# Kernel tuning notes

Measured on AMD Instinct MI355X. Metric: run time of the kernel, lower is better.

## Reference

```python
import jax, jax.numpy as jnp
import numpy as np

NEG_SLOPE = 0.2  # PyG GATv2Conv default negative_slope


def setup_inputs() -> dict:
    key = jax.random.key(0)
    ks = jax.random.split(key, 8)
    B, N, C, H, F, E = 16, 5000, 128, 2, 64, 1_280_000
    T = B * N
    s = 0.05
    x = jax.random.normal(ks[0], (B, N, C), jnp.float32)
    edge_index = jax.random.randint(ks[1], (2, E), 0, T, jnp.int32)
    Wl = jax.random.normal(ks[2], (C, H * F), jnp.float32) * s
    bl = jnp.zeros((H * F,), jnp.float32)
    Wr = jax.random.normal(ks[3], (C, H * F), jnp.float32) * s
    br = jnp.zeros((H * F,), jnp.float32)
    att = jax.random.normal(ks[4], (H, F), jnp.float32) * s
    bias = jnp.zeros((H * F,), jnp.float32)
    return {"x": x, "edge_index": edge_index, "Wl": Wl, "bl": bl,
            "Wr": Wr, "br": br, "att": att, "bias": bias}


def reference(x, edge_index, Wl, bl, Wr, br, att, bias):
    # x: (B, N, C) -> flatten to (T, C), T = B*N total nodes
    B, N, C = x.shape
    T = B * N
    H, F = att.shape
    xf = x.reshape(T, C)
    x_l = (xf @ Wl + bl).reshape(T, H, F)  # source transform (lin_l)
    x_r = (xf @ Wr + br).reshape(T, H, F)  # target transform (lin_r)
    # add self loops (add_self_loops=True)
    loops = jnp.arange(T, dtype=edge_index.dtype)
    src = jnp.concatenate([edge_index[0], loops])
    dst = jnp.concatenate([edge_index[1], loops])
    # GATv2 score: att . LeakyReLU(x_j + x_i)
    e = jax.nn.leaky_relu(x_l[src] + x_r[dst], NEG_SLOPE)  # (Et, H, F)
    logits = jnp.einsum('ehf,hf->eh', e, att)              # (Et, H)
    # edge softmax over incoming edges of each dst node
    m = jax.lax.stop_gradient(jax.ops.segment_max(logits, dst, num_segments=T))
    p = jnp.exp(logits - m[dst])
    denom = jax.ops.segment_sum(p, dst, num_segments=T)
    alpha = p / denom[dst]                                  # (Et, H)
    # aggregate: out_i = sum_j alpha_ij * x_l[j]
    out = jax.ops.segment_sum(x_l[src] * alpha[:, :, None], dst, num_segments=T)
    out = out.reshape(T, H * F) + bias  # concat=True -> (T, H*F)
    return out.reshape(B, N, H * F)
```

## Files before the change

kernel.cpp:

```cpp
#include <hip/hip_runtime.h>
#include <hip/hip_bf16.h>

typedef __hip_bfloat16 bf16;
typedef short s16x8 __attribute__((ext_vector_type(8)));
typedef float f32x4 __attribute__((ext_vector_type(4)));
typedef float f32x2 __attribute__((ext_vector_type(2)));

#define NEG_SLOPE 0.2f
#define MAXB 160
#define EPB  4096
#define CAP  12288

__device__ __forceinline__ unsigned int f32_to_bf16_bits(float f) {
    unsigned int u = __float_as_uint(f);
    return (u + 0x7FFFu + ((u >> 16) & 1u)) >> 16;
}
__device__ __forceinline__ float bf16lo_to_f32(unsigned int u) {
    return __uint_as_float(u << 16);
}
__device__ __forceinline__ float bf16hi_to_f32(unsigned int u) {
    return __uint_as_float(u & 0xFFFF0000u);
}
__device__ __forceinline__ float loadf_rt(const void* p, size_t i, int isb) {
    return isb ? __bfloat162float(((const bf16*)p)[i]) : ((const float*)p)[i];
}

#define ROR_ADD(v, n)                                                          \
    v += __int_as_float(__builtin_amdgcn_update_dpp(                           \
        0, __float_as_int(v), 0x120 + (n), 0xF, 0xF, true))

__global__ void prep_w(const unsigned short* __restrict__ xh,
                       const void* __restrict__ Wl, const void* __restrict__ Wr,
                       unsigned short* __restrict__ bpack,
                       int* __restrict__ flag, int* __restrict__ gtot)
{
    if (blockIdx.x == 16) {
        int tid = threadIdx.x;
        for (int j = tid; j < MAXB; j += 256) gtot[j] = 0;
        unsigned short h = xh[tid & 255];
        int e = (h >> 7) & 0xFF;
        int c = ((h & 0x7FFF) == 0 || (e >= 117 && e <= 131)) ? 1 : 0;
        __shared__ int sc[4];
        int lane = tid & 63, wid = tid >> 6;
        #pragma unroll
        for (int off = 32; off; off >>= 1) c += __shfl_xor(c, off, 64);
        if (lane == 0) sc[wid] = c;
        __syncthreads();
        if (tid == 0) *flag = ((sc[0] + sc[1] + sc[2] + sc[3]) >= 4 * 192) ? 1 : 0;
        return;
    }

    __shared__ int s_isb;
    {
        int tl = threadIdx.x;
        if (tl < 64) {
            int cnt = 0;
            for (int j = tl; j < 256; j += 64) {
                unsigned short h = xh[j];
                int e = (h >> 7) & 0xFF;
                if ((h & 0x7FFF) == 0 || (e >= 117 && e <= 131)) cnt++;
            }
            #pragma unroll
            for (int off = 32; off; off >>= 1) cnt += __shfl_xor(cnt, off, 64);
            if (tl == 0) s_isb = (cnt >= 192) ? 1 : 0;
        }
        __syncthreads();
    }
    int isb = s_isb;

    int tid = blockIdx.x * 256 + threadIdx.x;
    int lane = tid & 63;
    int kc   = (tid >> 6) & 3;
    int nt   = (tid >> 8) & 7;
    int mat  = tid >> 11;
    const void* W = mat ? Wr : Wl;
    int n  = nt * 16 + (lane & 15);
    int k0 = kc * 32 + (lane >> 4) * 8;
    unsigned short* o = bpack + (size_t)tid * 8;
    #pragma unroll
    for (int j = 0; j < 8; ++j)
        o[j] = (unsigned short)f32_to_bf16_bits(loadf_rt(W, (size_t)(k0 + j) * 128 + n, isb));
}

__global__ void gemm_or_hist(const void* __restrict__ x,
                             const unsigned short* __restrict__ bpack,
                             const void* __restrict__ bl, const void* __restrict__ br,
                             unsigned int* __restrict__ xlp, unsigned int* __restrict__ xrp,
                             int T, const int* __restrict__ flag,
                             const int* __restrict__ ei, int E, int Et,
                             int nbuck, int Gg, int* __restrict__ gtot)
{
    __shared__ int h[4][MAXB];

    if ((int)blockIdx.x >= Gg) {
        int hb  = blockIdx.x - Gg;
        int tid = threadIdx.x, wid = tid >> 6;
        for (int j = tid; j < 4 * MAXB; j += 256) h[j / MAXB][j % MAXB] = 0;
        __syncthreads();
        int start = hb * EPB;
        int end   = min(start + EPB, Et);
        for (int i = start + tid; i < end; i += 256) {
            int dst = (i < E) ? ei[E + i] : (i - E);
            atomicAdd(&h[wid][dst >> 9], 1);
        }
        __syncthreads();
        for (int b = tid; b < nbuck; b += 256) {
            int v = h[0][b] + h[1][b] + h[2][b] + h[3][b];
            if (v) atomicAdd(&gtot[b], v);
        }
        return;
    }

    int isb  = *flag;
    int lane = threadIdx.x & 63;
    int w    = blockIdx.x * 4 + (threadIdx.x >> 6);
    int row0 = w * 16;
    if (row0 >= T) return;
    int m = lane & 15, quad = lane >> 4;
    int arow = min(row0 + m, T - 1);

    f32x4 acc[16];
    #pragma unroll
    for (int nt = 0; nt < 16; ++nt) acc[nt] = (f32x4){0.f, 0.f, 0.f, 0.f};

    const s16x8* bp = (const s16x8*)bpack;
    for (int kc = 0; kc < 4; ++kc) {
        s16x8 a;
        if (isb) {
            const unsigned short* xb = (const unsigned short*)x
                                     + (size_t)arow * 128 + kc * 32 + quad * 8;
            a = *(const s16x8*)xb;
        } else {
            const float* xp = (const float*)x + (size_t)arow * 128 + kc * 32 + quad * 8;
            float4 xa = ((const float4*)xp)[0];
            float4 xc = ((const float4*)xp)[1];
            a[0] = (short)f32_to_bf16_bits(xa.x); a[1] = (short)f32_to_bf16_bits(xa.y);
            a[2] = (short)f32_to_bf16_bits(xa.z); a[3] = (short)f32_to_bf16_bits(xa.w);
            a[4] = (short)f32_to_bf16_bits(xc.x); a[5] = (short)f32_to_bf16_bits(xc.y);
            a[6] = (short)f32_to_bf16_bits(xc.z); a[7] = (short)f32_to_bf16_bits(xc.w);
        }
        #pragma unroll
        for (int nt = 0; nt < 16; ++nt) {
            s16x8 b = bp[(size_t)(((nt >> 3) * 32) + (nt & 7) * 4 + kc) * 64 + lane];
            acc[nt] = __builtin_amdgcn_mfma_f32_16x16x32_bf16(a, b, acc[nt], 0, 0, 0);
        }
    }
    #pragma unroll
    for (int nt = 0; nt < 4; ++nt) {
        int fl = nt * 16 + m;
        float bl0 = loadf_rt(bl, fl, isb), bl1 = loadf_rt(bl, 64 + fl, isb);
        float br0 = loadf_rt(br, fl, isb), br1 = loadf_rt(br, 64 + fl, isb);
        #pragma unroll
        for (int r = 0; r < 4; ++r) {
            int t = row0 + quad * 4 + r;
            if (t < T) {
                unsigned int pl = f32_to_bf16_bits(acc[nt][r] + bl0)
                                | (f32_to_bf16_bits(acc[nt + 4][r] + bl1) << 16);
                unsigned int pr = f32_to_bf16_bits(acc[nt + 8][r] + br0)
                                | (f32_to_bf16_bits(acc[nt + 12][r] + br1) << 16);
                xlp[(size_t)t * 64 + fl] = pl;
                xrp[(size_t)t * 64 + fl] = pr;
            }
        }
    }
}

__global__ void scan_buckets(int* __restrict__ gtot, int nbuck, int Et,
                             int* __restrict__ bases, int* __restrict__ rowptr_T)
{
    __shared__ int sd[256];
    int tid = threadIdx.x;
    int v = (tid < nbuck) ? gtot[tid] : 0;
    sd[tid] = v;
    __syncthreads();
    for (int off = 1; off < 256; off <<= 1) {
        int u = (tid >= off) ? sd[tid - off] : 0;
        __syncthreads();
        sd[tid] += u;
        __syncthreads();
    }
    int excl = sd[tid] - v;
    if (tid < nbuck) { bases[tid] = excl; gtot[tid] = excl; }
    if (tid == 0) { bases[nbuck] = Et; *rowptr_T = Et; }
}

__global__ void bucket_scatter2(const int* __restrict__ ei, int E, int Et,
                                int nbuck, int* __restrict__ gcur,
                                unsigned int* __restrict__ packed)
{
    __shared__ int h[4][MAXB];
    __shared__ int cur[MAXB];
    int tid = threadIdx.x, wid = tid >> 6;
    for (int j = tid; j < 4 * MAXB; j += 256) h[j / MAXB][j % MAXB] = 0;
    __syncthreads();
    int start = blockIdx.x * EPB;
    int end   = min(start + EPB, Et);
    for (int i = start + tid; i < end; i += 256) {
        int dst = (i < E) ? ei[E + i] : (i - E);
        atomicAdd(&h[wid][dst >> 9], 1);
    }
    __syncthreads();
    for (int b = tid; b < nbuck; b += 256) {
        int v = h[0][b] + h[1][b] + h[2][b] + h[3][b];
        cur[b] = v ? atomicAdd(&gcur[b], v) : 0;
    }
    __syncthreads();
    for (int i = start + tid; i < end; i += 256) {
        int src, dst;
        if (i < E) { src = ei[i]; dst = ei[E + i]; }
        else       { src = i - E; dst = i - E; }
        int pos = atomicAdd(&cur[dst >> 9], 1);
        packed[pos] = ((unsigned int)src << 9) | (unsigned int)(dst & 511);
    }
}

__global__ void build_csr(unsigned int* __restrict__ colpacked,
                          const int* __restrict__ bases, int nbuck,
                          int Et, int T, int* __restrict__ row_ptr)
{
    __shared__ unsigned int st[CAP];
    __shared__ int h[512];
    __shared__ int off[512];
    __shared__ int ws[4];
    int b    = blockIdx.x;
    int tid  = threadIdx.x, lane = tid & 63, wid = tid >> 6;
    int base = bases[b];
    int endb = bases[b + 1];
    int m    = min(endb - base, CAP);

    for (int i = tid; i < m; i += 256) st[i] = colpacked[base + i];
    for (int j = tid; j < 512; j += 256) h[j] = 0;
    __syncthreads();
    for (int i = tid; i < m; i += 256) atomicAdd(&h[st[i] & 511], 1);
    __syncthreads();

    int h0 = h[2 * tid], h1 = h[2 * tid + 1];
    int s  = h0 + h1;
    int xx = s;
    #pragma unroll
    for (int o = 1; o < 64; o <<= 1) {
        int u = __shfl_up(xx, o, 64);
        if (lane >= o) xx += u;
    }
    if (lane == 63) ws[wid] = xx;
    __syncthreads();
    int wo = 0;
    for (int wv = 0; wv < 4; ++wv) if (wv < wid) wo += ws[wv];
    int e0 = wo + xx - s;
    int e1 = e0 + h0;
    off[2 * tid]     = e0;
    off[2 * tid + 1] = e1;
    int node0 = b * 512 + 2 * tid;
    if (node0 < T)     row_ptr[node0]     = base + e0;
    if (node0 + 1 < T) row_ptr[node0 + 1] = base + e1;
    __syncthreads();

    for (int i = tid; i < m; i += 256) {
        unsigned int p = st[i];
        int pos = atomicAdd(&off[p & 511], 1);
        colpacked[base + pos] = p >> 9;
    }
}

__global__ void aggregate(const unsigned int* __restrict__ xlp,
                          const unsigned int* __restrict__ xrp,
                          const int* __restrict__ row_ptr, const int* __restrict__ col,
                          const void* __restrict__ att, const void* __restrict__ bias,
                          float* __restrict__ out, int T,
                          const int* __restrict__ flag)
{
    int lane = threadIdx.x & 63;
    int node = blockIdx.x * 8 + (threadIdx.x >> 5);
    if (node >= T) return;
    int isb = *flag;
    int g = (lane >> 4) & 1;
    int q = lane & 15;

    uint4 xr4 = ((const uint4*)(xrp + (size_t)node * 64))[q];
    f32x2 xr2[4], at2[4];
    {
        unsigned int xrw[4] = {xr4.x, xr4.y, xr4.z, xr4.w};
        const float LOG2E = 1.44269504f;
        #pragma unroll
        for (int k = 0; k < 4; ++k) {
            xr2[k] = (f32x2){bf16lo_to_f32(xrw[k]), bf16hi_to_f32(xrw[k])};
            at2[k] = (f32x2){loadf_rt(att, q * 4 + k, isb) * LOG2E,
                             loadf_rt(att, 64 + q * 4 + k, isb) * LOG2E};
        }
    }

    f32x2 s2 = {0.f, 0.f};
    f32x2 a2[4] = {{0.f, 0.f}, {0.f, 0.f}, {0.f, 0.f}, {0.f, 0.f}};

    int beg = row_ptr[node], end = row_ptr[node + 1];

    bool v0 = (beg + g) < end;      int sA = v0 ? col[beg + g]     : node;
    bool v1 = (beg + 2 + g) < end;  int sB = v1 ? col[beg + 2 + g] : node;
    bool v2 = (beg + 4 + g) < end;  int sC = v2 ? col[beg + 4 + g] : node;
    uint4 cx = ((const uint4*)(xlp + (size_t)sA * 64))[q];
    uint4 nx = ((const uint4*)(xlp + (size_t)sB * 64))[q];

    for (int i = beg; i < end; i += 2) {
        bool v3 = (i + 6 + g) < end;
        int  sD = v3 ? col[i + 6 + g] : node;
        uint4 px = ((const uint4*)(xlp + (size_t)sC * 64))[q];

        unsigned int xlw[4] = {cx.x, cx.y, cx.z, cx.w};
        f32x2 xl2[4];
        f32x2 t2 = {0.f, 0.f};
        #pragma unroll
        for (int k = 0; k < 4; ++k) {
            xl2[k] = (f32x2){bf16lo_to_f32(xlw[k]), bf16hi_to_f32(xlw[k])};
            f32x2 e  = xl2[k] + xr2[k];
            f32x2 lr = __builtin_elementwise_max(e, e * NEG_SLOPE);
            t2 = __builtin_elementwise_fma(lr, at2[k], t2);
        }
        float t0 = t2.x, t1 = t2.y;
        ROR_ADD(t0, 8); ROR_ADD(t1, 8);
        ROR_ADD(t0, 4); ROR_ADD(t1, 4);
        ROR_ADD(t0, 2); ROR_ADD(t1, 2);
        ROR_ADD(t0, 1); ROR_ADD(t1, 1);
        t0 = fminf(t0, 43.3f);
        t1 = fminf(t1, 43.3f);
        f32x2 p2;
        p2.x = v0 ? exp2f(t0) : 0.f;
        p2.y = v0 ? exp2f(t1) : 0.f;
        s2 += p2;
        #pragma unroll
        for (int k = 0; k < 4; ++k)
            a2[k] = __builtin_elementwise_fma(p2, xl2[k], a2[k]);

        cx = nx; nx = px;
        v0 = v1; v1 = v2; v2 = v3; sC = sD;
    }

    s2.x += __shfl_xor(s2.x, 16, 64);
    s2.y += __shfl_xor(s2.y, 16, 64);
    #pragma unroll
    for (int k = 0; k < 4; ++k) {
        a2[k].x += __shfl_xor(a2[k].x, 16, 64);
        a2[k].y += __shfl_xor(a2[k].y, 16, 64);
    }

    float inv0 = (s2.x > 0.f) ? 1.f / s2.x : 0.f;
    float inv1 = (s2.y > 0.f) ? 1.f / s2.y : 0.f;
    if (g == 0) {
        float4 o;
        o.x = fmaf(a2[0].x, inv0, loadf_rt(bias, q * 4 + 0, isb));
        o.y = fmaf(a2[1].x, inv0, loadf_rt(bias, q * 4 + 1, isb));
        o.z = fmaf(a2[2].x, inv0, loadf_rt(bias, q * 4 + 2, isb));
        o.w = fmaf(a2[3].x, inv0, loadf_rt(bias, q * 4 + 3, isb));
        ((float4*)(out + (size_t)node * 128))[q] = o;
    } else {
        float4 o;
        o.x = fmaf(a2[0].y, inv1, loadf_rt(bias, 64 + q * 4 + 0, isb));
        o.y = fmaf(a2[1].y, inv1, loadf_rt(bias, 64 + q * 4 + 1, isb));
        o.z = fmaf(a2[2].y, inv1, loadf_rt(bias, 64 + q * 4 + 2, isb));
        o.w = fmaf(a2[3].y, inv1, loadf_rt(bias, 64 + q * 4 + 3, isb));
        ((float4*)(out + (size_t)node * 128))[16 + q] = o;
    }
}

extern "C" void kernel_launch(void* const* d_in, const int* in_sizes, int n_in,
                              void* d_out, int out_size, void* d_ws, size_t ws_size,
                              hipStream_t stream)
{
    const void* x    = d_in[0];
    const int*  ei   = (const int*)d_in[1];
    const void* Wl   = d_in[2];
    const void* bl   = d_in[3];
    const void* Wr   = d_in[4];
    const void* br   = d_in[5];
    const void* att  = d_in[6];
    const void* bias = d_in[7];
    float* out = (float*)d_out;

    int T     = in_sizes[0] / 128;
    int E     = in_sizes[1] / 2;
    int Et    = E + T;
    int nbuck = (T + 511) >> 9;
    int nb    = (Et + EPB - 1) / EPB;
    int Gg    = (T + 63) / 64;

    char* w = (char*)d_ws;
    unsigned int* xlp = (unsigned int*)w;  w += (size_t)T * 64 * 4;
    unsigned int* xrp = (unsigned int*)w;  w += (size_t)T * 64 * 4;
    int* rowptr = (int*)w;  w += (size_t)(T + 1) * 4;
    unsigned int* col = (unsigned int*)w;  w += (size_t)Et * 4;
    int* gtot   = (int*)w;  w += MAXB * 4;
    int* bases  = (int*)w;  w += (MAXB + 8) * 4;
    int* flag   = (int*)w;  w += 256;
    unsigned short* bpack = (unsigned short*)w;  w += 2 * 8 * 4 * 64 * 8 * 2;

    prep_w<<<17, 256, 0, stream>>>((const unsigned short*)x, Wl, Wr, bpack, flag, gtot);
    gemm_or_hist<<<Gg + nb, 256, 0, stream>>>(x, bpack, bl, br, xlp, xrp, T, flag,
                                              ei, E, Et, nbuck, Gg, gtot);
    scan_buckets<<<1, 256, 0, stream>>>(gtot, nbuck, Et, bases, rowptr + T);
    bucket_scatter2<<<nb, 256, 0, stream>>>(ei, E, Et, nbuck, gtot, col);
    build_csr<<<nbuck, 256, 0, stream>>>(col, bases, nbuck, Et, T, rowptr);

    aggregate<<<(T + 7) / 8, 256, 0, stream>>>(xlp, xrp, rowptr, (const int*)col,
                                               att, bias, out, T, flag);
}
```

Measured before the change: 241.7 us.

## Fold bucket scan into scatter and CSR kernels; stage GEMM stores through LDS

Removes the single-block scan_buckets launch. Each bucket_scatter2 block and each build_csr block now recomputes the 160-entry prefix scan locally, and a separate delta array holds the per-bucket atomic cursors. The GEMM epilogue also writes results to a shared-memory transpose tile and then emits 16-byte coalesced row stores instead of scattered 4-byte stores. The cost is a redundant per-block scan with extra syncs and about 33KB more LDS in gemm_or_hist, which may reduce occupancy for the histogram blocks too.

```diff
diff --git a/kernel.cpp b/kernel.cpp
--- a/kernel.cpp
+++ b/kernel.cpp
@@ -10,6 +10,7 @@
 #define MAXB 160
 #define EPB  4096
 #define CAP  12288
+#define TRS  132
 
 __device__ __forceinline__ unsigned int f32_to_bf16_bits(float f) {
     unsigned int u = __float_as_uint(f);
@@ -32,11 +33,11 @@
 __global__ void prep_w(const unsigned short* __restrict__ xh,
                        const void* __restrict__ Wl, const void* __restrict__ Wr,
                        unsigned short* __restrict__ bpack,
-                       int* __restrict__ flag, int* __restrict__ gtot)
+                       int* __restrict__ flag, int* __restrict__ g2)
 {
     if (blockIdx.x == 16) {
         int tid = threadIdx.x;
-        for (int j = tid; j < MAXB; j += 256) gtot[j] = 0;
+        for (int j = tid; j < 2 * MAXB; j += 256) g2[j] = 0;
         unsigned short h = xh[tid & 255];
         int e = (h >> 7) & 0xFF;
         int c = ((h & 0x7FFF) == 0 || (e >= 117 && e <= 131)) ? 1 : 0;
@@ -91,6 +92,7 @@
                              int nbuck, int Gg, int* __restrict__ gtot)
 {
     __shared__ int h[4][MAXB];
+    __shared__ unsigned int tr[4][16][TRS];
 
     if ((int)blockIdx.x >= Gg) {
         int hb  = blockIdx.x - Gg;
@@ -113,7 +115,8 @@
 
     int isb  = *flag;
     int lane = threadIdx.x & 63;
-    int w    = blockIdx.x * 4 + (threadIdx.x >> 6);
+    int wv   = threadIdx.x >> 6;
+    int w    = blockIdx.x * 4 + wv;
     int row0 = w * 16;
     if (row0 >= T) return;
     int m = lane & 15, quad = lane >> 4;
@@ -145,6 +148,7 @@
             acc[nt] = __builtin_amdgcn_mfma_f32_16x16x32_bf16(a, b, acc[nt], 0, 0, 0);
         }
     }
+
     #pragma unroll
     for (int nt = 0; nt < 4; ++nt) {
         int fl = nt * 16 + m;
@@ -152,24 +156,38 @@
         float br0 = loadf_rt(br, fl, isb), br1 = loadf_rt(br, 64 + fl, isb);
         #pragma unroll
         for (int r = 0; r < 4; ++r) {
-            int t = row0 + quad * 4 + r;
-            if (t < T) {
-                unsigned int pl = f32_to_bf16_bits(acc[nt][r] + bl0)
-                                | (f32_to_bf16_bits(acc[nt + 4][r] + bl1) << 16);
-                unsigned int pr = f32_to_bf16_bits(acc[nt + 8][r] + br0)
-                                | (f32_to_bf16_bits(acc[nt + 12][r] + br1) << 16);
-                xlp[(size_t)t * 64 + fl] = pl;
-                xrp[(size_t)t * 64 + fl] = pr;
-            }
-        }
-    }
-}
-
-__global__ void scan_buckets(int* __restrict__ gtot, int nbuck, int Et,
-                             int* __restrict__ bases, int* __restrict__ rowptr_T)
-{
+            unsigned int pl = f32_to_bf16_bits(acc[nt][r] + bl0)
+                            | (f32_to_bf16_bits(acc[nt + 4][r] + bl1) << 16);
+            unsigned int pr = f32_to_bf16_bits(acc[nt + 8][r] + br0)
+                            | (f32_to_bf16_bits(acc[nt + 12][r] + br1) << 16);
+            tr[wv][quad * 4 + r][fl]      = pl;
+            tr[wv][quad * 4 + r][64 + fl] = pr;
+        }
+    }
+    #pragma unroll
+    for (int s = 0; s < 4; ++s) {
+        int rr = s * 4 + quad;
+        int t  = row0 + rr;
+        if (t < T) {
+            int c4 = m;
+            uint4 vl = *(const uint4*)&tr[wv][rr][c4 * 4];
+            uint4 vr = *(const uint4*)&tr[wv][rr][64 + c4 * 4];
+            ((uint4*)(xlp + (size_t)t * 64))[c4] = vl;
+            ((uint4*)(xrp + (size_t)t * 64))[c4] = vr;
+        }
+    }
+}
+
+__global__ void bucket_scatter2(const int* __restrict__ ei, int E, int Et,
+                                int nbuck, const int* __restrict__ gtot,
+                                int* __restrict__ delta,
+                                unsigned int* __restrict__ packed)
+{
+    __shared__ int h[4][MAXB];
+    __shared__ int cur[MAXB];
     __shared__ int sd[256];
-    int tid = threadIdx.x;
+    int tid = threadIdx.x, wid = tid >> 6;
+    for (int j = tid; j < 4 * MAXB; j += 256) h[j / MAXB][j % MAXB] = 0;
     int v = (tid < nbuck) ? gtot[tid] : 0;
     sd[tid] = v;
     __syncthreads();
@@ -180,19 +198,7 @@
         __syncthreads();
     }
     int excl = sd[tid] - v;
-    if (tid < nbuck) { bases[tid] = excl; gtot[tid] = excl; }
-    if (tid == 0) { bases[nbuck] = Et; *rowptr_T = Et; }
-}
-
-__global__ void bucket_scatter2(const int* __restrict__ ei, int E, int Et,
-                                int nbuck, int* __restrict__ gcur,
-                                unsigned int* __restrict__ packed)
-{
-    __shared__ int h[4][MAXB];
-    __shared__ int cur[MAXB];
-    int tid = threadIdx.x, wid = tid >> 6;
-    for (int j = tid; j < 4 * MAXB; j += 256) h[j / MAXB][j % MAXB] = 0;
-    __syncthreads();
+
     int start = blockIdx.x * EPB;
     int end   = min(start + EPB, Et);
     for (int i = start + tid; i < end; i += 256) {
@@ -200,9 +206,9 @@
         atomicAdd(&h[wid][dst >> 9], 1);
     }
     __syncthreads();
-    for (int b = tid; b < nbuck; b += 256) {
-        int v = h[0][b] + h[1][b] + h[2][b] + h[3][b];
-        cur[b] = v ? atomicAdd(&gcur[b], v) : 0;
+    if (tid < nbuck) {
+        int c = h[0][tid] + h[1][tid] + h[2][tid] + h[3][tid];
+        cur[tid] = excl + (c ? atomicAdd(&delta[tid], c) : 0);
     }
     __syncthreads();
     for (int i = start + tid; i < end; i += 256) {
@@ -215,17 +221,31 @@
 }
 
 __global__ void build_csr(unsigned int* __restrict__ colpacked,
-                          const int* __restrict__ bases, int nbuck,
+                          const int* __restrict__ gtot, int nbuck,
                           int Et, int T, int* __restrict__ row_ptr)
 {
     __shared__ unsigned int st[CAP];
     __shared__ int h[512];
     __shared__ int off[512];
     __shared__ int ws[4];
+    __shared__ int sd[256];
+    __shared__ int sb2[2];
     int b    = blockIdx.x;
     int tid  = threadIdx.x, lane = tid & 63, wid = tid >> 6;
-    int base = bases[b];
-    int endb = bases[b + 1];
+
+    int v = (tid < nbuck) ? gtot[tid] : 0;
+    sd[tid] = v;
+    __syncthreads();
+    for (int o = 1; o < 256; o <<= 1) {
+        int u = (tid >= o) ? sd[tid - o] : 0;
+        __syncthreads();
+        sd[tid] += u;
+        __syncthreads();
+    }
+    if (tid == b) { sb2[0] = sd[tid] - v; sb2[1] = sd[tid]; }
+    __syncthreads();
+    int base = sb2[0];
+    int endb = sb2[1];
     int m    = min(endb - base, CAP);
 
     for (int i = tid; i < m; i += 256) st[i] = colpacked[base + i];
@@ -253,6 +273,7 @@
     int node0 = b * 512 + 2 * tid;
     if (node0 < T)     row_ptr[node0]     = base + e0;
     if (node0 + 1 < T) row_ptr[node0 + 1] = base + e1;
+    if (b == nbuck - 1 && tid == 0) row_ptr[T] = Et;
     __syncthreads();
 
     for (int i = tid; i < m; i += 256) {
@@ -387,17 +408,17 @@
     unsigned int* xrp = (unsigned int*)w;  w += (size_t)T * 64 * 4;
     int* rowptr = (int*)w;  w += (size_t)(T + 1) * 4;
     unsigned int* col = (unsigned int*)w;  w += (size_t)Et * 4;
-    int* gtot   = (int*)w;  w += MAXB * 4;
-    int* bases  = (int*)w;  w += (MAXB + 8) * 4;
+    int* g2     = (int*)w;  w += 2 * MAXB * 4;
     int* flag   = (int*)w;  w += 256;
     unsigned short* bpack = (unsigned short*)w;  w += 2 * 8 * 4 * 64 * 8 * 2;
-
-    prep_w<<<17, 256, 0, stream>>>((const unsigned short*)x, Wl, Wr, bpack, flag, gtot);
+    int* gtot  = g2;
+    int* delta = g2 + MAXB;
+
+    prep_w<<<17, 256, 0, stream>>>((const unsigned short*)x, Wl, Wr, bpack, flag, g2);
     gemm_or_hist<<<Gg + nb, 256, 0, stream>>>(x, bpack, bl, br, xlp, xrp, T, flag,
                                               ei, E, Et, nbuck, Gg, gtot);
-    scan_buckets<<<1, 256, 0, stream>>>(gtot, nbuck, Et, bases, rowptr + T);
-    bucket_scatter2<<<nb, 256, 0, stream>>>(ei, E, Et, nbuck, gtot, col);
-    build_csr<<<nbuck, 256, 0, stream>>>(col, bases, nbuck, Et, T, rowptr);
+    bucket_scatter2<<<nb, 256, 0, stream>>>(ei, E, Et, nbuck, gtot, delta, col);
+    build_csr<<<nbuck, 256, 0, stream>>>(col, gtot, nbuck, Et, T, rowptr);
 
     aggregate<<<(T + 7) / 8, 256, 0, stream>>>(xlp, xrp, rowptr, (const int*)col,
                                                att, bias, out, T, flag);
```

Result: no change. 238.7 us (-1.2%).
